# Kernel tuning notes

Measured on AMD Instinct MI355X. Metric: run time of the kernel, lower is better.

Reference implementation:

```python
import jax, jax.numpy as jnp
import numpy as np

B, D = 8192, 256
NUM_CLASSES = 128
CHUNK = 256          # matches module chunk_size; B % CHUNK == 0
TEMP = 0.07
EPS_NORM = 1e-12


def setup_inputs() -> dict:
    key = jax.random.key(0)
    k1, k2 = jax.random.split(key)
    features = jax.random.normal(k1, (B, D), dtype=jnp.float32)
    labels = jax.random.randint(k2, (B,), 0, NUM_CLASSES, dtype=jnp.int64)
    return {"features": features, "labels": labels}


def reference(features, labels):
    n = features.shape[0]
    temperature = max(TEMP, 1e-4)

    # F.normalize(dim=1): x / max(||x||, eps)
    norm = jnp.maximum(jnp.linalg.norm(features, axis=1, keepdims=True), EPS_NORM)
    f = features / norm
    # clamp is a no-op after normalization but kept for faithfulness
    f = jnp.clip(f, -1000.0, 1000.0)

    # [B, B] similarity; the torch loop computes exactly these rows chunk by chunk
    sim = jnp.matmul(f, f.T) / temperature

    # self-mask: each row i masks column i (diagonal of its chunk's square block)
    self_mask = ~jnp.eye(n, dtype=bool)

    # positive mask: same label, excluding self
    pos = (labels[:, None] == labels[None, :]) & self_mask
    # per-chunk fallback: if a 256-row chunk has no positives at all, use self_mask
    pos_c = pos.reshape(n // CHUNK, CHUNK, n)
    has_pos = pos_c.any(axis=(1, 2), keepdims=True)
    pos = jnp.where(has_pos, pos_c, self_mask.reshape(n // CHUNK, CHUNK, n)).reshape(n, n)

    # max-subtract BEFORE self-masking (faithful: includes self-sim = 1/temp)
    sim_max = jnp.max(sim, axis=1, keepdims=True)
    logits = jnp.clip(sim - jax.lax.stop_gradient(sim_max), -1000.0, 1000.0)

    exp_sim = jnp.maximum(jnp.exp(logits), 1e-8) * self_mask
    log_sum_exp = jnp.log(jnp.sum(exp_sim, axis=1, keepdims=True) + 1e-8)
    log_prob = jnp.maximum(logits - log_sum_exp, -1000.0)

    pos_pairs = jnp.sum(pos, axis=1)                      # [B] int
    row_loss = -jnp.sum(pos * log_prob, axis=1)           # [B]
    valid = pos_pairs > 0
    row_loss = jnp.where(valid, row_loss / jnp.maximum(pos_pairs, 1).astype(row_loss.dtype), 0.0)

    total_loss = jnp.sum(row_loss)
    total_pairs = jnp.sum(valid).astype(jnp.float32)
    mean_loss = total_loss / (total_pairs + 1e-8)
    loss = mean_loss  # reduction == 'mean'
    return loss, total_pairs, mean_loss
```

## Files before the change

### kernel.cpp

```cpp
#include <hip/hip_runtime.h>
#include <hip/hip_bf16.h>
#include <type_traits>

#define NB 8192
#define DD 256
#define INV_T (1.0f/0.07f)
#define LOG2E 1.4426950408889634f
#define K1    (INV_T*LOG2E)
#define CEXP  6.2087204553847255e-7f
#define NSTRIP 32
#define TILE 256
#define BN 64
#define NITER 4
#define BUFB (BN*DD*2)
#define NTILES (NSTRIP*(NSTRIP+1)/2)

typedef __attribute__((ext_vector_type(8))) short s8v;
typedef __attribute__((ext_vector_type(4))) float f4v;
typedef unsigned int u32;
typedef unsigned short u16;

#define OFF_FB   0
#define OFF_SE   (4*1024*1024)
#define OFF_SP   (OFF_SE + NSTRIP*NB*4)
#define OFF_CL   (OFF_SP + NSTRIP*NB*4)
#define OFF_CV   (OFF_CL + 256)
#define OFF_CNT  (OFF_CV + 256)

__device__ __forceinline__ u32 packEP(float e, float p) {
    __hip_bfloat16 be = __float2bfloat16(e), bp = __float2bfloat16(p);
    return (u32)*(u16*)&be | ((u32)*(u16*)&bp << 16);
}
__device__ __forceinline__ float unpLo(u32 x) {
    u16 h = (u16)x; __hip_bfloat16 b = *(__hip_bfloat16*)&h; return __bfloat162float(b);
}
__device__ __forceinline__ float unpHi(u32 x) {
    u16 h = (u16)(x >> 16); __hip_bfloat16 b = *(__hip_bfloat16*)&h; return __bfloat162float(b);
}

__global__ void k_norm(const float* __restrict__ feat,
                       __hip_bfloat16* __restrict__ fb, int* __restrict__ cnt) {
    if (blockIdx.x == 0 && threadIdx.x == 0) *cnt = 0;
    const int t = threadIdx.x;
    const int w = t >> 6, l = t & 63;
    const int row = blockIdx.x * 4 + w;
    const float4 v = ((const float4*)feat)[row * 64 + l];
    float s = v.x * v.x + v.y * v.y + v.z * v.z + v.w * v.w;
    #pragma unroll
    for (int d = 32; d; d >>= 1) s += __shfl_xor(s, d, 64);
    const float scale = 1.0f / fmaxf(sqrtf(s), 1e-12f);
    __hip_bfloat16 h0 = __float2bfloat16(v.x * scale);
    __hip_bfloat16 h1 = __float2bfloat16(v.y * scale);
    __hip_bfloat16 h2 = __float2bfloat16(v.z * scale);
    __hip_bfloat16 h3 = __float2bfloat16(v.w * scale);
    ushort4 o;
    o.x = *(u16*)&h0; o.y = *(u16*)&h1; o.z = *(u16*)&h2; o.w = *(u16*)&h3;
    ((ushort4*)fb)[row * 64 + l] = o;
}

__device__ __forceinline__ void gld16(const void* g, void* l) {
    __builtin_amdgcn_global_load_lds((const __attribute__((address_space(1))) u32*)g,
                                     (__attribute__((address_space(3))) u32*)l, 16, 0, 0);
}

__launch_bounds__(512)
__global__ void k_main(const __hip_bfloat16* __restrict__ fb,
                       const int* __restrict__ lab,
                       float* __restrict__ SE, float* __restrict__ SP) {
    __shared__ __align__(16) char ldsB[2 * BUFB];
    __shared__ int ldsLab[TILE];
    __shared__ u32 ldsCol[8][NITER][BN];
    const int tid = threadIdx.x;
    const int w = tid >> 6;
    const int l = tid & 63;
    const int l15 = l & 15, lg = l >> 4;

    int cb = 0, rem = blockIdx.x;
    while (rem >= NSTRIP - cb) { rem -= NSTRIP - cb; cb++; }
    const int rb = cb + rem;
    const int row0 = rb * TILE, col0 = cb * TILE;
    const int wbase = row0 + w * 32;

    if (tid < TILE) ldsLab[tid] = lab[col0 + tid];

    s8v a[2][8];
    #pragma unroll
    for (int m = 0; m < 2; m++)
        #pragma unroll
        for (int kk = 0; kk < 8; kk++)
            a[m][kk] = *(const s8v*)(fb + (wbase + m * 16 + l15) * DD + kk * 32 + lg * 8);

    int labr[8];
    #pragma unroll
    for (int m = 0; m < 2; m++)
        #pragma unroll
        for (int r = 0; r < 4; r++)
            labr[m * 4 + r] = lab[wbase + m * 16 + lg * 4 + r];

    float sE[8], sPa[8];
    #pragma unroll
    for (int i = 0; i < 8; i++) { sE[i] = 0.f; sPa[i] = 0.f; }

    auto stage = [&](int ct, int bufoff) {
        const char* gt = (const char*)fb + (size_t)(col0 + ct * BN) * (DD * 2);
        #pragma unroll
        for (int i = 0; i < 4; i++) {
            const int x = i * 8192 + (tid << 4);
            const int br = x >> 9;
            const int inrow = x & 511;
            gld16(gt + br * 512 + (inrow ^ ((br & 7) << 4)),
                  ldsB + bufoff + i * 8192 + w * 1024);
        }
    };

    auto run = [&](auto diagC) {
        constexpr bool DIAG = decltype(diagC)::value;
        stage(0, 0);
        __syncthreads();
        for (int ct = 0; ct < NITER; ct++) {
            const int curoff = (ct & 1) * BUFB;
            if (ct + 1 < NITER) stage(ct + 1, curoff ^ BUFB);

            int lc[4];
            #pragma unroll
            for (int n = 0; n < 4; n++)
                lc[n] = ldsLab[ct * BN + n * 16 + l15];

            f4v acc[2][4];
            #pragma unroll
            for (int m = 0; m < 2; m++)
                #pragma unroll
                for (int n = 0; n < 4; n++)
                    acc[m][n] = (f4v){0.f, 0.f, 0.f, 0.f};

            #pragma unroll
            for (int kk = 0; kk < 8; kk++) {
                s8v bfr[4];
                #pragma unroll
                for (int n = 0; n < 4; n++) {
                    const int br = n * 16 + l15;
                    const int ad = (br * 512 + kk * 64 + lg * 16) ^ ((br & 7) << 4);
                    bfr[n] = *(const s8v*)(ldsB + curoff + ad);
                }
                #pragma unroll
                for (int m = 0; m < 2; m++)
                    #pragma unroll
                    for (int n = 0; n < 4; n++)
                        acc[m][n] = __builtin_amdgcn_mfma_f32_16x16x32_bf16(a[m][kk], bfr[n], acc[m][n], 0, 0, 0);
            }

            float cE[4], cP[4];
            #pragma unroll
            for (int n = 0; n < 4; n++) { cE[n] = 0.f; cP[n] = 0.f; }
            #pragma unroll
            for (int n = 0; n < 4; n++) {
                #pragma unroll
                for (int m = 0; m < 2; m++)
                    #pragma unroll
                    for (int r = 0; r < 4; r++) {
                        const int idx = m * 4 + r;
                        const float v = acc[m][n][r];
                        float e = exp2f(v * K1);
                        bool pos = (lc[n] == labr[idx]);
                        if (DIAG) {
                            const int row = wbase + m * 16 + lg * 4 + r;
                            const int coln = col0 + ct * BN + n * 16 + l15;
                            const bool nself = (row != coln);
                            e = nself ? e : 0.f;
                            pos = pos && nself;
                        }
                        const float pv = pos ? v : 0.f;
                        sE[idx] += e;
                        sPa[idx] += pv;
                        if (!DIAG) { cE[n] += e; cP[n] += pv; }
                    }
            }

            if (!DIAG) {
                #pragma unroll
                for (int n = 0; n < 4; n++) {
                    cE[n] += __shfl_xor(cE[n], 16, 64);
                    cE[n] += __shfl_xor(cE[n], 32, 64);
                    cP[n] += __shfl_xor(cP[n], 16, 64);
                    cP[n] += __shfl_xor(cP[n], 32, 64);
                }
                if (l < 16) {
                    #pragma unroll
                    for (int n = 0; n < 4; n++)
                        ldsCol[w][ct][n * 16 + l15] = packEP(cE[n], cP[n]);
                }
            }
            __syncthreads();
        }
    };
    if (rb == cb) run(std::true_type{}); else run(std::false_type{});

    #pragma unroll
    for (int idx = 0; idx < 8; idx++) {
        #pragma unroll
        for (int d = 1; d < 16; d <<= 1) {
            sE[idx]  += __shfl_xor(sE[idx], d, 16);
            sPa[idx] += __shfl_xor(sPa[idx], d, 16);
        }
    }
    if (l15 == 0) {
        #pragma unroll
        for (int idx = 0; idx < 8; idx++) {
            const int row = wbase + (idx >> 2) * 16 + lg * 4 + (idx & 3);
            SE[cb * NB + row] = sE[idx];
            SP[cb * NB + row] = sPa[idx];
        }
    }

    if (rb != cb && tid < TILE) {
        const int ct = tid >> 6, j = tid & 63;
        float e = 0.f, p = 0.f;
        #pragma unroll
        for (int w2 = 0; w2 < 8; w2++) {
            const u32 x = ldsCol[w2][ct][j];
            e += unpLo(x);
            p += unpHi(x);
        }
        SE[rb * NB + col0 + tid] = e;
        SP[rb * NB + col0 + tid] = p;
    }
}

__global__ void k_rows(const int* __restrict__ lab,
                       const float* __restrict__ SE, const float* __restrict__ SP,
                       float* __restrict__ CL, float* __restrict__ CV,
                       int* __restrict__ cnt, float* __restrict__ out) {
    __shared__ int h[128];
    const int t = threadIdx.x;
    if (t < 128) h[t] = 0;
    __syncthreads();
    #pragma unroll
    for (int i = 0; i < 32; i++)
        atomicAdd(&h[lab[t + i * 256]], 1);
    __syncthreads();

    const int row = blockIdx.x * 256 + t;
    float se = 0.f, spa = 0.f;
    #pragma unroll
    for (int s = 0; s < NSTRIP; s++) {
        se  += SE[s * NB + row];
        spa += SP[s * NB + row];
    }
    const int n = h[lab[row]] - 1;
    const float lse = logf(se * CEXP + 1e-8f);
    const bool valid = n > 0;
    float loss = valid ? (lse - (spa - (float)n) * INV_T / (float)n) : 0.f;
    float vf = valid ? 1.f : 0.f;
    #pragma unroll
    for (int d = 32; d; d >>= 1) { loss += __shfl_xor(loss, d, 64); vf += __shfl_xor(vf, d, 64); }
    __shared__ float pl[4], pv[4];
    __shared__ int isLast;
    if ((t & 63) == 0) { pl[t >> 6] = loss; pv[t >> 6] = vf; }
    __syncthreads();
    if (t == 0) {
        CL[blockIdx.x] = pl[0] + pl[1] + pl[2] + pl[3];
        CV[blockIdx.x] = pv[0] + pv[1] + pv[2] + pv[3];
        __threadfence();
        isLast = (atomicAdd(cnt, 1) == 31);
    }
    __syncthreads();
    if (isLast) {
        __threadfence();
        float lsum = (t < 32) ? CL[t] : 0.f;
        float vsum = (t < 32) ? CV[t] : 0.f;
        #pragma unroll
        for (int d = 32; d; d >>= 1) { lsum += __shfl_xor(lsum, d, 64); vsum += __shfl_xor(vsum, d, 64); }
        if (t == 0) {
            const float mean = lsum / (vsum + 1e-8f);
            out[0] = mean;
            out[1] = vsum;
            out[2] = mean;
        }
    }
}

extern "C" void kernel_launch(void* const* d_in, const int* in_sizes, int n_in,
                              void* d_out, int out_size, void* d_ws, size_t ws_size,
                              hipStream_t stream) {
    (void)in_sizes; (void)n_in; (void)out_size; (void)ws_size;
    const float* feat = (const float*)d_in[0];
    const int*   lab  = (const int*)d_in[1];
    char* ws = (char*)d_ws;
    __hip_bfloat16* fb = (__hip_bfloat16*)(ws + OFF_FB);
    float* SE = (float*)(ws + OFF_SE);
    float* SP = (float*)(ws + OFF_SP);
    float* CL = (float*)(ws + OFF_CL);
    float* CV = (float*)(ws + OFF_CV);
    int*   cnt = (int*)(ws + OFF_CNT);
    float* out = (float*)d_out;

    hipLaunchKernelGGL(k_norm, dim3(NB / 4), dim3(256), 0, stream, feat, fb, cnt);
    hipLaunchKernelGGL(k_main, dim3(NTILES), dim3(512), 0, stream, fb, lab, SE, SP);
    hipLaunchKernelGGL(k_rows, dim3(NB / 256), dim3(256), 0, stream, lab, SE, SP, CL, CV, cnt, out);
}
```

Measured before the change: 75.87 us.

## Rebalance triangular tile schedule with paired strips and atomic row accumulation

Replaces the one-block-per-triangle-tile grid with 256 blocks that each process an equal slice of paired row strips (s and 31-s), so each block gets a near-equal number of 64-column sub-tiles. Row sums are accumulated via atomics into zero-initialised buffers, while column sums are written per row strip and reduced in the final kernel. It aims to remove tail imbalance and wave quantisation, at the cost of extra barriers per sub-tile, global label reads, and atomics.

```diff
diff --git a/kernel.cpp b/kernel.cpp
--- a/kernel.cpp
+++ b/kernel.cpp
@@ -1,6 +1,5 @@
 #include <hip/hip_runtime.h>
 #include <hip/hip_bf16.h>
-#include <type_traits>
 
 #define NB 8192
 #define DD 256
@@ -11,9 +10,7 @@
 #define NSTRIP 32
 #define TILE 256
 #define BN 64
-#define NITER 4
 #define BUFB (BN*DD*2)
-#define NTILES (NSTRIP*(NSTRIP+1)/2)
 
 typedef __attribute__((ext_vector_type(8))) short s8v;
 typedef __attribute__((ext_vector_type(4))) float f4v;
@@ -21,27 +18,20 @@
 typedef unsigned short u16;
 
 #define OFF_FB   0
-#define OFF_SE   (4*1024*1024)
-#define OFF_SP   (OFF_SE + NSTRIP*NB*4)
-#define OFF_CL   (OFF_SP + NSTRIP*NB*4)
+#define OFF_SEA  (4*1024*1024)
+#define OFF_SPA  (OFF_SEA + NB*4)
+#define OFF_CE   (OFF_SPA + NB*4)
+#define OFF_CP   (OFF_CE + NSTRIP*NB*4)
+#define OFF_CL   (OFF_CP + NSTRIP*NB*4)
 #define OFF_CV   (OFF_CL + 256)
 #define OFF_CNT  (OFF_CV + 256)
 
-__device__ __forceinline__ u32 packEP(float e, float p) {
-    __hip_bfloat16 be = __float2bfloat16(e), bp = __float2bfloat16(p);
-    return (u32)*(u16*)&be | ((u32)*(u16*)&bp << 16);
-}
-__device__ __forceinline__ float unpLo(u32 x) {
-    u16 h = (u16)x; __hip_bfloat16 b = *(__hip_bfloat16*)&h; return __bfloat162float(b);
-}
-__device__ __forceinline__ float unpHi(u32 x) {
-    u16 h = (u16)(x >> 16); __hip_bfloat16 b = *(__hip_bfloat16*)&h; return __bfloat162float(b);
-}
-
 __global__ void k_norm(const float* __restrict__ feat,
-                       __hip_bfloat16* __restrict__ fb, int* __restrict__ cnt) {
-    if (blockIdx.x == 0 && threadIdx.x == 0) *cnt = 0;
+                       __hip_bfloat16* __restrict__ fb,
+                       float* __restrict__ SEa, int* __restrict__ cnt) {
     const int t = threadIdx.x;
+    if (blockIdx.x == 0 && t == 0) *cnt = 0;
+    if (blockIdx.x < 64) SEa[blockIdx.x * 256 + t] = 0.f;
     const int w = t >> 6, l = t & 63;
     const int row = blockIdx.x * 4 + w;
     const float4 v = ((const float4*)feat)[row * 64 + l];
@@ -66,43 +56,66 @@
 __launch_bounds__(512)
 __global__ void k_main(const __hip_bfloat16* __restrict__ fb,
                        const int* __restrict__ lab,
-                       float* __restrict__ SE, float* __restrict__ SP) {
+                       float* __restrict__ SEa, float* __restrict__ SPa,
+                       float* __restrict__ CE, float* __restrict__ CP) {
     __shared__ __align__(16) char ldsB[2 * BUFB];
-    __shared__ int ldsLab[TILE];
-    __shared__ u32 ldsCol[8][NITER][BN];
+    __shared__ float ldsColE[8][BN];
+    __shared__ float ldsColP[8][BN];
     const int tid = threadIdx.x;
     const int w = tid >> 6;
     const int l = tid & 63;
     const int l15 = l & 15, lg = l >> 4;
 
-    int cb = 0, rem = blockIdx.x;
-    while (rem >= NSTRIP - cb) { rem -= NSTRIP - cb; cb++; }
-    const int rb = cb + rem;
-    const int row0 = rb * TILE, col0 = cb * TILE;
-    const int wbase = row0 + w * 32;
-
-    if (tid < TILE) ldsLab[tid] = lab[col0 + tid];
+    const int s = blockIdx.x >> 4;
+    const int j = blockIdx.x & 15;
+    const int nA = 4 * (32 - s);
+    const int cnt = 8 + (j >= 12 ? 1 : 0);
+    const int off = 8 * j + (j > 12 ? j - 12 : 0);
 
     s8v a[2][8];
+    int labr[8];
+    int wbase = 0;
+    auto loadA = [&](int r) {
+        wbase = r * TILE + w * 32;
+        #pragma unroll
+        for (int m = 0; m < 2; m++)
+            #pragma unroll
+            for (int kk = 0; kk < 8; kk++)
+                a[m][kk] = *(const s8v*)(fb + (wbase + m * 16 + l15) * DD + kk * 32 + lg * 8);
+        #pragma unroll
+        for (int m = 0; m < 2; m++)
+            #pragma unroll
+            for (int r2 = 0; r2 < 4; r2++)
+                labr[m * 4 + r2] = lab[wbase + m * 16 + lg * 4 + r2];
+    };
+
+    float sE[8], sPa_[8];
     #pragma unroll
-    for (int m = 0; m < 2; m++)
-        #pragma unroll
-        for (int kk = 0; kk < 8; kk++)
-            a[m][kk] = *(const s8v*)(fb + (wbase + m * 16 + l15) * DD + kk * 32 + lg * 8);
-
-    int labr[8];
-    #pragma unroll
-    for (int m = 0; m < 2; m++)
-        #pragma unroll
-        for (int r = 0; r < 4; r++)
-            labr[m * 4 + r] = lab[wbase + m * 16 + lg * 4 + r];
-
-    float sE[8], sPa[8];
-    #pragma unroll
-    for (int i = 0; i < 8; i++) { sE[i] = 0.f; sPa[i] = 0.f; }
-
-    auto stage = [&](int ct, int bufoff) {
-        const char* gt = (const char*)fb + (size_t)(col0 + ct * BN) * (DD * 2);
+    for (int i = 0; i < 8; i++) { sE[i] = 0.f; sPa_[i] = 0.f; }
+    auto flushRows = [&]() {
+        #pragma unroll
+        for (int idx = 0; idx < 8; idx++) {
+            #pragma unroll
+            for (int d = 1; d < 16; d <<= 1) {
+                sE[idx]   += __shfl_xor(sE[idx], d, 16);
+                sPa_[idx] += __shfl_xor(sPa_[idx], d, 16);
+            }
+        }
+        if (l15 == 0) {
+            #pragma unroll
+            for (int idx = 0; idx < 8; idx++) {
+                const int row = wbase + (idx >> 2) * 16 + lg * 4 + (idx & 3);
+                atomicAdd(&SEa[row], sE[idx]);
+                atomicAdd(&SPa[row], sPa_[idx]);
+            }
+        }
+        #pragma unroll
+        for (int i = 0; i < 8; i++) { sE[i] = 0.f; sPa_[i] = 0.f; }
+    };
+
+    auto stage = [&](int g, int bufoff) {
+        const int c0 = (g < nA ? g : g - nA) * 64;
+        const char* gt = (const char*)fb + (size_t)c0 * (DD * 2);
         #pragma unroll
         for (int i = 0; i < 4; i++) {
             const int x = i * 8192 + (tid << 4);
@@ -113,121 +126,113 @@
         }
     };
 
-    auto run = [&](auto diagC) {
-        constexpr bool DIAG = decltype(diagC)::value;
-        stage(0, 0);
-        __syncthreads();
-        for (int ct = 0; ct < NITER; ct++) {
-            const int curoff = (ct & 1) * BUFB;
-            if (ct + 1 < NITER) stage(ct + 1, curoff ^ BUFB);
-
-            int lc[4];
+    stage(off, 0);
+    loadA(off < nA ? 31 - s : s);
+    __syncthreads();
+
+    for (int t = 0; t < cnt; t++) {
+        const int g = off + t;
+        const int curoff = (t & 1) * BUFB;
+        if (t + 1 < cnt) stage(g + 1, curoff ^ BUFB);
+
+        const int r = (g < nA) ? 31 - s : s;
+        const int i = (g < nA) ? g : g - nA;
+        const int col0 = i * 64;
+        const bool diag = ((i >> 2) == r);
+
+        int lc[4];
+        #pragma unroll
+        for (int n = 0; n < 4; n++)
+            lc[n] = lab[col0 + n * 16 + l15];
+
+        f4v acc[2][4];
+        #pragma unroll
+        for (int m = 0; m < 2; m++)
             #pragma unroll
             for (int n = 0; n < 4; n++)
-                lc[n] = ldsLab[ct * BN + n * 16 + l15];
-
-            f4v acc[2][4];
+                acc[m][n] = (f4v){0.f, 0.f, 0.f, 0.f};
+
+        #pragma unroll
+        for (int kk = 0; kk < 8; kk++) {
+            s8v bfr[4];
+            #pragma unroll
+            for (int n = 0; n < 4; n++) {
+                const int br = n * 16 + l15;
+                const int ad = (br * 512 + kk * 64 + lg * 16) ^ ((br & 7) << 4);
+                bfr[n] = *(const s8v*)(ldsB + curoff + ad);
+            }
             #pragma unroll
             for (int m = 0; m < 2; m++)
                 #pragma unroll
                 for (int n = 0; n < 4; n++)
-                    acc[m][n] = (f4v){0.f, 0.f, 0.f, 0.f};
-
-            #pragma unroll
-            for (int kk = 0; kk < 8; kk++) {
-                s8v bfr[4];
+                    acc[m][n] = __builtin_amdgcn_mfma_f32_16x16x32_bf16(a[m][kk], bfr[n], acc[m][n], 0, 0, 0);
+        }
+
+        float cE[4], cP[4];
+        #pragma unroll
+        for (int n = 0; n < 4; n++) { cE[n] = 0.f; cP[n] = 0.f; }
+        #pragma unroll
+        for (int n = 0; n < 4; n++) {
+            #pragma unroll
+            for (int m = 0; m < 2; m++)
+                #pragma unroll
+                for (int rr = 0; rr < 4; rr++) {
+                    const int idx = m * 4 + rr;
+                    const float v = acc[m][n][rr];
+                    float e = exp2f(v * K1);
+                    bool pos = (lc[n] == labr[idx]);
+                    if (diag) {
+                        const int row = wbase + m * 16 + lg * 4 + rr;
+                        const int coln = col0 + n * 16 + l15;
+                        const bool nself = (row != coln);
+                        e = nself ? e : 0.f;
+                        pos = pos && nself;
+                    }
+                    const float pv = pos ? v : 0.f;
+                    sE[idx] += e;
+                    sPa_[idx] += pv;
+                    cE[n] += e;
+                    cP[n] += pv;
+                }
+        }
+
+        if (!diag) {
+            #pragma unroll
+            for (int n = 0; n < 4; n++) {
+                cE[n] += __shfl_xor(cE[n], 16, 64);
+                cE[n] += __shfl_xor(cE[n], 32, 64);
+                cP[n] += __shfl_xor(cP[n], 16, 64);
+                cP[n] += __shfl_xor(cP[n], 32, 64);
+            }
+            if (l < 16) {
                 #pragma unroll
                 for (int n = 0; n < 4; n++) {
-                    const int br = n * 16 + l15;
-                    const int ad = (br * 512 + kk * 64 + lg * 16) ^ ((br & 7) << 4);
-                    bfr[n] = *(const s8v*)(ldsB + curoff + ad);
+                    ldsColE[w][n * 16 + l15] = cE[n];
+                    ldsColP[w][n * 16 + l15] = cP[n];
                 }
-                #pragma unroll
-                for (int m = 0; m < 2; m++)
-                    #pragma unroll
-                    for (int n = 0; n < 4; n++)
-                        acc[m][n] = __builtin_amdgcn_mfma_f32_16x16x32_bf16(a[m][kk], bfr[n], acc[m][n], 0, 0, 0);
-            }
-
-            float cE[4], cP[4];
-            #pragma unroll
-            for (int n = 0; n < 4; n++) { cE[n] = 0.f; cP[n] = 0.f; }
-            #pragma unroll
-            for (int n = 0; n < 4; n++) {
-                #pragma unroll
-                for (int m = 0; m < 2; m++)
-                    #pragma unroll
-                    for (int r = 0; r < 4; r++) {
-                        const int idx = m * 4 + r;
-                        const float v = acc[m][n][r];
-                        float e = exp2f(v * K1);
-                        bool pos = (lc[n] == labr[idx]);
-                        if (DIAG) {
-                            const int row = wbase + m * 16 + lg * 4 + r;
-                            const int coln = col0 + ct * BN + n * 16 + l15;
-                            const bool nself = (row != coln);
-                            e = nself ? e : 0.f;
-                            pos = pos && nself;
-                        }
-                        const float pv = pos ? v : 0.f;
-                        sE[idx] += e;
-                        sPa[idx] += pv;
-                        if (!DIAG) { cE[n] += e; cP[n] += pv; }
-                    }
-            }
-
-            if (!DIAG) {
-                #pragma unroll
-                for (int n = 0; n < 4; n++) {
-                    cE[n] += __shfl_xor(cE[n], 16, 64);
-                    cE[n] += __shfl_xor(cE[n], 32, 64);
-                    cP[n] += __shfl_xor(cP[n], 16, 64);
-                    cP[n] += __shfl_xor(cP[n], 32, 64);
-                }
-                if (l < 16) {
-                    #pragma unroll
-                    for (int n = 0; n < 4; n++)
-                        ldsCol[w][ct][n * 16 + l15] = packEP(cE[n], cP[n]);
-                }
-            }
-            __syncthreads();
-        }
-    };
-    if (rb == cb) run(std::true_type{}); else run(std::false_type{});
-
-    #pragma unroll
-    for (int idx = 0; idx < 8; idx++) {
-        #pragma unroll
-        for (int d = 1; d < 16; d <<= 1) {
-            sE[idx]  += __shfl_xor(sE[idx], d, 16);
-            sPa[idx] += __shfl_xor(sPa[idx], d, 16);
+            }
+        }
+        __syncthreads();
+        if (!diag && tid < BN) {
+            float e = 0.f, p = 0.f;
+            #pragma unroll
+            for (int w2 = 0; w2 < 8; w2++) { e += ldsColE[w2][tid]; p += ldsColP[w2][tid]; }
+            CE[r * NB + col0 + tid] = e;
+            CP[r * NB + col0 + tid] = p;
+        }
+        __syncthreads();
+
+        if (t + 1 < cnt && g + 1 == nA) {
+            flushRows();
+            loadA(s);
         }
     }
-    if (l15 == 0) {
-        #pragma unroll
-        for (int idx = 0; idx < 8; idx++) {
-            const int row = wbase + (idx >> 2) * 16 + lg * 4 + (idx & 3);
-            SE[cb * NB + row] = sE[idx];
-            SP[cb * NB + row] = sPa[idx];
-        }
-    }
-
-    if (rb != cb && tid < TILE) {
-        const int ct = tid >> 6, j = tid & 63;
-        float e = 0.f, p = 0.f;
-        #pragma unroll
-        for (int w2 = 0; w2 < 8; w2++) {
-            const u32 x = ldsCol[w2][ct][j];
-            e += unpLo(x);
-            p += unpHi(x);
-        }
-        SE[rb * NB + col0 + tid] = e;
-        SP[rb * NB + col0 + tid] = p;
-    }
+    flushRows();
 }
 
 __global__ void k_rows(const int* __restrict__ lab,
-                       const float* __restrict__ SE, const float* __restrict__ SP,
+                       const float* __restrict__ SEa, const float* __restrict__ SPa,
+                       const float* __restrict__ CE, const float* __restrict__ CP,
                        float* __restrict__ CL, float* __restrict__ CV,
                        int* __restrict__ cnt, float* __restrict__ out) {
     __shared__ int h[128];
@@ -240,11 +245,10 @@
     __syncthreads();
 
     const int row = blockIdx.x * 256 + t;
-    float se = 0.f, spa = 0.f;
-    #pragma unroll
-    for (int s = 0; s < NSTRIP; s++) {
-        se  += SE[s * NB + row];
-        spa += SP[s * NB + row];
+    float se = SEa[row], spa = SPa[row];
+    for (int r = blockIdx.x + 1; r < NSTRIP; r++) {
+        se  += CE[r * NB + row];
+        spa += CP[r * NB + row];
     }
     const int n = h[lab[row]] - 1;
     const float lse = logf(se * CEXP + 1e-8f);
@@ -287,14 +291,16 @@
     const int*   lab  = (const int*)d_in[1];
     char* ws = (char*)d_ws;
     __hip_bfloat16* fb = (__hip_bfloat16*)(ws + OFF_FB);
-    float* SE = (float*)(ws + OFF_SE);
-    float* SP = (float*)(ws + OFF_SP);
-    float* CL = (float*)(ws + OFF_CL);
-    float* CV = (float*)(ws + OFF_CV);
+    float* SEa = (float*)(ws + OFF_SEA);
+    float* SPa = (float*)(ws + OFF_SPA);
+    float* CE  = (float*)(ws + OFF_CE);
+    float* CP  = (float*)(ws + OFF_CP);
+    float* CL  = (float*)(ws + OFF_CL);
+    float* CV  = (float*)(ws + OFF_CV);
     int*   cnt = (int*)(ws + OFF_CNT);
     float* out = (float*)d_out;
 
-    hipLaunchKernelGGL(k_norm, dim3(NB / 4), dim3(256), 0, stream, feat, fb, cnt);
-    hipLaunchKernelGGL(k_main, dim3(NTILES), dim3(512), 0, stream, fb, lab, SE, SP);
-    hipLaunchKernelGGL(k_rows, dim3(NB / 256), dim3(256), 0, stream, lab, SE, SP, CL, CV, cnt, out);
-}
+    hipLaunchKernelGGL(k_norm, dim3(NB / 4), dim3(256), 0, stream, feat, fb, SEa, cnt);
+    hipLaunchKernelGGL(k_main, dim3(256), dim3(512), 0, stream, fb, lab, SEa, SPa, CE, CP);
+    hipLaunchKernelGGL(k_rows, dim3(NB / 256), dim3(256), 0, stream, lab, SEa, SPa, CE, CP, CL, CV, cnt, out);
+}
```

Measured after the change: 71.64 us. -5.6%, faster.
